# Performance work log

Hardware: AMD Instinct MI355X
Metric: run time of the kernel (lower is better)

## Reference

```python
import jax, jax.numpy as jnp
import numpy as np

B, S, D, H = 2, 2048, 1024, 16
DK = D // H

def setup_inputs() -> dict:
    key = jax.random.key(0)
    ks = jax.random.split(key, 12)
    def lin(k, shape, fan_in):
        bound = 1.0 / np.sqrt(fan_in)
        return jax.random.uniform(k, shape, jnp.float32, -bound, bound)
    inp = {
        'Q': jax.random.normal(ks[0], (B, S, D), jnp.float32),
        'K': jax.random.normal(ks[1], (B, S, D), jnp.float32),
        'V': jax.random.normal(ks[2], (B, S, D), jnp.float32),
        # padding mask: last 128 key positions of batch element 0 are padding
        'padding_mask': jnp.ones((B, 1, 1, S), jnp.int32).at[0, :, :, -128:].set(0),
        # causal look-ahead mask
        'look_ahead_mask': jnp.tril(jnp.ones((S, S), jnp.int32))[None, None],
        'Wq': lin(ks[3], (D, D), D), 'bq': lin(ks[4], (D,), D),
        'Wk': lin(ks[5], (D, D), D), 'bk': lin(ks[6], (D,), D),
        'Wv': lin(ks[7], (D, D), D), 'bv': lin(ks[8], (D,), D),
        'Wo': lin(ks[9], (D, D), D), 'bo': lin(ks[10], (D,), D),
    }
    return inp

def _split_heads(x):
    # [B,S,D] -> [B,H,S,DK]
    b, s, _ = x.shape
    return x.reshape(b, s, H, DK).transpose(0, 2, 1, 3)

def reference(Q, K, V, padding_mask, look_ahead_mask, Wq, bq, Wk, bk, Wv, bv, Wo, bo):
    q = _split_heads(Q @ Wq.T + bq)  # [B,H,S,DK]
    k = _split_heads(K @ Wk.T + bk)
    v = _split_heads(V @ Wv.T + bv)
    scores = jnp.einsum('bhqd,bhkd->bhqk', q, k) / np.sqrt(DK).astype(np.float32)
    neg_inf = jnp.float32(-jnp.inf)
    scores = jnp.where(padding_mask == 0, neg_inf, scores)
    scores = jnp.where(look_ahead_mask == 0, neg_inf, scores)
    weights = jax.nn.softmax(scores, axis=-1)  # dropout is identity in eval mode
    x = jnp.einsum('bhqk,bhkd->bhqd', weights, v)  # [B,H,S,DK]
    x = x.transpose(0, 2, 1, 3).reshape(Q.shape[0], Q.shape[1], D)
    return x @ Wo.T + bo
```

## Files before the change

### kernel.cpp

```cpp
#include <hip/hip_runtime.h>
#include <hip/hip_bf16.h>

#define B_   2
#define S_   2048
#define D_   1024
#define H_   16
#define DK_  64

typedef unsigned short u16;
typedef __attribute__((ext_vector_type(8))) short bf16x8;
typedef __attribute__((ext_vector_type(4))) float f32x4;

#define CHUNK_   12
#define NSLOT_   48

static __device__ __forceinline__ u16 f2bf(float f) {
  union { float f; unsigned u; } v; v.f = f;
  unsigned r = v.u + 0x7FFF + ((v.u >> 16) & 1);
  return (u16)(r >> 16);
}

static __device__ __forceinline__ void gl_lds16(const void* g, void* l) {
  __builtin_amdgcn_global_load_lds(
      (const __attribute__((address_space(1))) void*)g,
      (__attribute__((address_space(3))) void*)l, 16, 0, 0);
}

__global__ void cvt7(const float4* __restrict__ i0, const float4* __restrict__ i1,
                     const float4* __restrict__ i2, const float4* __restrict__ i3,
                     const float4* __restrict__ i4, const float4* __restrict__ i5,
                     const float4* __restrict__ i6,
                     ushort4* __restrict__ o0, ushort4* __restrict__ o1,
                     ushort4* __restrict__ o2, ushort4* __restrict__ o3,
                     ushort4* __restrict__ o4, ushort4* __restrict__ o5,
                     ushort4* __restrict__ o6, int nbig, int nsmall) {
  int y = blockIdx.y;
  const float4* in; ushort4* out; int bound;
  switch (y) {
    case 0: in = i0; out = o0; bound = nbig; break;
    case 1: in = i1; out = o1; bound = nbig; break;
    case 2: in = i2; out = o2; bound = nbig; break;
    case 3: in = i3; out = o3; bound = nsmall; break;
    case 4: in = i4; out = o4; bound = nsmall; break;
    case 5: in = i5; out = o5; bound = nsmall; break;
    default: in = i6; out = o6; bound = nsmall; break;
  }
  int i = blockIdx.x * blockDim.x + threadIdx.x;
  if (i < bound) {
    float4 v = in[i];
    ushort4 r;
    r.x = f2bf(v.x); r.y = f2bf(v.y); r.z = f2bf(v.z); r.w = f2bf(v.w);
    out[i] = r;
  }
}

__launch_bounds__(256, 3)
__global__ void gemm_qkv(const u16* __restrict__ Xq, const u16* __restrict__ Xk, const u16* __restrict__ Xv,
                         const u16* __restrict__ Wq, const u16* __restrict__ Wk, const u16* __restrict__ Wv,
                         const float* __restrict__ bq, const float* __restrict__ bk, const float* __restrict__ bv,
                         u16* __restrict__ outq, u16* __restrict__ outk, u16* __restrict__ outv) {
  const int z = blockIdx.z;
  const u16* Am; const u16* Bm; int m0, n0;
  if (z == 2) { Am = Wv; Bm = Xv; m0 = blockIdx.x * 128; n0 = blockIdx.y * 128; }
  else if (z == 1) { Am = Xk; Bm = Wk; m0 = blockIdx.y * 128; n0 = blockIdx.x * 128; }
  else { Am = Xq; Bm = Wq; m0 = blockIdx.y * 128; n0 = blockIdx.x * 128; }
  const float* bias = (z == 0) ? bq : (z == 1) ? bk : bv;

  __shared__ __align__(16) u16 As[128 * 64];
  __shared__ __align__(16) u16 Bs[128 * 64];

  const int tid = threadIdx.x, lane = tid & 63, w = tid >> 6;
  const int q = lane >> 4, cl = lane & 15;
  const int wr = w >> 1, wc = w & 1;

  f32x4 acc[4][4] = {};

  for (int k0 = 0; k0 < D_; k0 += 64) {
#pragma unroll
    for (int i = 0; i < 4; ++i) {
      int ch = i * 256 + tid;
      int row = ch >> 3, c = ch & 7;
      int gc = (c ^ (row & 7)) << 3;
      gl_lds16(Am + (size_t)(m0 + row) * D_ + k0 + gc, As + ch * 8);
      gl_lds16(Bm + (size_t)(n0 + row) * D_ + k0 + gc, Bs + ch * 8);
    }
    __syncthreads();

#pragma unroll
    for (int kk = 0; kk < 2; ++kk) {
      bf16x8 af[4], bfr[4];
      int jc = (kk << 2) | q;
#pragma unroll
      for (int r = 0; r < 4; ++r)
        af[r]  = *(const bf16x8*)(As + (wr * 64 + r * 16 + cl) * 64 + ((jc ^ (cl & 7)) << 3));
#pragma unroll
      for (int c = 0; c < 4; ++c)
        bfr[c] = *(const bf16x8*)(Bs + (wc * 64 + c * 16 + cl) * 64 + ((jc ^ (cl & 7)) << 3));
#pragma unroll
      for (int r = 0; r < 4; ++r)
#pragma unroll
        for (int c = 0; c < 4; ++c)
          acc[r][c] = __builtin_amdgcn_mfma_f32_16x16x32_bf16(af[r], bfr[c], acc[r][c], 0, 0, 0);
    }
    __syncthreads();
  }

  if (z == 2) {
#pragma unroll
    for (int r = 0; r < 4; ++r) {
#pragma unroll
      for (int rr = 0; rr < 4; ++rr) {
        int j = m0 + wr * 64 + r * 16 + q * 4 + rr;
        float bval = bias[j];
        int hh = j >> 6, dk = j & 63;
#pragma unroll
        for (int c = 0; c < 4; ++c) {
          int n = n0 + wc * 64 + c * 16 + cl;
          int bb = n >> 11, s = n & (S_ - 1);
          outv[((size_t)(bb * H_ + hh) * DK_ + dk) * S_ + s] = f2bf(acc[r][c][rr] + bval);
        }
      }
    }
  } else {
    const float scale = (z == 0) ? 0.125f : 1.0f;
    u16* o = (z == 0) ? outq : outk;
#pragma unroll
    for (int c = 0; c < 4; ++c) {
      int j = n0 + wc * 64 + c * 16 + cl;
      float bval = bias[j];
      int hh = j >> 6, dk = j & 63;
#pragma unroll
      for (int r = 0; r < 4; ++r) {
#pragma unroll
        for (int rr = 0; rr < 4; ++rr) {
          int n = m0 + wr * 64 + r * 16 + q * 4 + rr;
          int bb = n >> 11, s = n & (S_ - 1);
          o[((size_t)(bb * H_ + hh) * S_ + s) * DK_ + dk] = f2bf((acc[r][c][rr] + bval) * scale);
        }
      }
    }
  }
}

__launch_bounds__(256, 4)
__global__ void attn(const u16* __restrict__ qh, const u16* __restrict__ kh,
                     const u16* __restrict__ vt, const int* __restrict__ pad,
                     u16* __restrict__ attn_out, float* __restrict__ Po, float* __restrict__ Pl) {
  __shared__ __align__(16) u16 Ks[64 * 64];
  __shared__ __align__(16) u16 Vs[64 * 64];
  __shared__ __align__(16) u16 Ps[4][16 * 72];
  __shared__ float Kbias[64];

  const int tid = threadIdx.x, lane = tid & 63, w = tid >> 6;
  const int q = lane >> 4, cl = lane & 15;
  const int h = blockIdx.y, b = blockIdx.z;

  const int x = blockIdx.x;
  int qt, ch, nch;
  if (x < 24)      { qt = 24 + x / 3;          ch = x % 3;       nch = 3; }
  else if (x < 48) { int y = x - 24; qt = 12 + y / 2; ch = y & 1; nch = 2; }
  else             { qt = x - 48;              ch = 0;           nch = 1; }
  const int qb = qt * 64;
  const int t0 = ch * CHUNK_;
  const int t1 = (qt < t0 + CHUNK_ - 1) ? qt : (t0 + CHUNK_ - 1);

  const u16* Q = qh + (size_t)(b * H_ + h) * S_ * DK_;
  const u16* K = kh + (size_t)(b * H_ + h) * S_ * DK_;
  const u16* V = vt + (size_t)(b * H_ + h) * DK_ * S_;
  const int* pm = pad + b * S_;

  const int qr0 = qb + w * 16;
  bf16x8 qf0 = *(const bf16x8*)(Q + (qr0 + cl) * DK_ + q * 8);
  bf16x8 qf1 = *(const bf16x8*)(Q + (qr0 + cl) * DK_ + 32 + q * 8);

  f32x4 o[4] = {};
  float ls[4] = {0.f, 0.f, 0.f, 0.f};
  u16* Pw = Ps[w];

  for (int it = t0; it <= t1; ++it) {
    const int kb = it << 6;
#pragma unroll
    for (int i = 0; i < 2; ++i) {
      int s = (i * 4 + w) * 64 + lane;
      int row = s >> 3;
      int c = (s & 7) ^ (row & 7);
      gl_lds16(K + (size_t)(kb + row) * DK_ + (c << 3), Ks + (size_t)s * 8);
      gl_lds16(V + (size_t)row * S_ + kb + (c << 3), Vs + (size_t)s * 8);
    }
    if (tid < 64) {
      Kbias[tid] = (pm[kb + tid] != 0) ? -6.0f : -3e38f;
    }
    __syncthreads();

    f32x4 sa[4];
#pragma unroll
    for (int ct = 0; ct < 4; ++ct) {
      int rk = ct * 16 + cl;
      int c0 = q ^ (rk & 7);
      bf16x8 kf0 = *(const bf16x8*)(Ks + rk * 64 + (c0 << 3));
      bf16x8 kf1 = *(const bf16x8*)(Ks + rk * 64 + ((c0 ^ 4) << 3));
      f32x4 zz = {};
      zz = __builtin_amdgcn_mfma_f32_16x16x32_bf16(qf0, kf0, zz, 0, 0, 0);
      zz = __builtin_amdgcn_mfma_f32_16x16x32_bf16(qf1, kf1, zz, 0, 0, 0);
      sa[ct] = zz;
    }

    if (it < qt) {
#pragma unroll
      for (int ct = 0; ct < 4; ++ct) {
        float kbv = Kbias[ct * 16 + cl];
#pragma unroll
        for (int rr = 0; rr < 4; ++rr) {
          float p = __expf(sa[ct][rr] + kbv);
          ls[rr] += p;
          Pw[(q * 4 + rr) * 72 + ct * 16 + cl] = f2bf(p);
        }
      }
    } else {
#pragma unroll
      for (int ct = 0; ct < 4; ++ct) {
        int kg = kb + ct * 16 + cl;
        float kbv = Kbias[ct * 16 + cl];
#pragma unroll
        for (int rr = 0; rr < 4; ++rr) {
          int qg = qr0 + q * 4 + rr;
          float p = (kg <= qg) ? __expf(sa[ct][rr] + kbv) : 0.f;
          ls[rr] += p;
          Pw[(q * 4 + rr) * 72 + ct * 16 + cl] = f2bf(p);
        }
      }
    }

    bf16x8 pf0 = *(const bf16x8*)(Pw + cl * 72 + q * 8);
    bf16x8 pf1 = *(const bf16x8*)(Pw + cl * 72 + 32 + q * 8);

#pragma unroll
    for (int ct = 0; ct < 4; ++ct) {
      int rv = ct * 16 + cl;
      int c0 = q ^ (rv & 7);
      bf16x8 vf0 = *(const bf16x8*)(Vs + rv * 64 + (c0 << 3));
      bf16x8 vf1 = *(const bf16x8*)(Vs + rv * 64 + ((c0 ^ 4) << 3));
      o[ct] = __builtin_amdgcn_mfma_f32_16x16x32_bf16(pf0, vf0, o[ct], 0, 0, 0);
      o[ct] = __builtin_amdgcn_mfma_f32_16x16x32_bf16(pf1, vf1, o[ct], 0, 0, 0);
    }
    __syncthreads();
  }

  if (nch == 1) {
#pragma unroll
    for (int rr = 0; rr < 4; ++rr) {
      float l = ls[rr];
      l += __shfl_xor(l, 1, 64);
      l += __shfl_xor(l, 2, 64);
      l += __shfl_xor(l, 4, 64);
      l += __shfl_xor(l, 8, 64);
      float inv = 1.0f / l;
      int qg = qr0 + q * 4 + rr;
      size_t base = (size_t)(b * S_ + qg) * D_ + h * DK_;
#pragma unroll
      for (int ct = 0; ct < 4; ++ct)
        attn_out[base + ct * 16 + cl] = f2bf(o[ct][rr] * inv);
    }
  } else {
    int pq = qt - 12;
    int off = (pq < 12) ? pq * 2 : 24 + (pq - 12) * 3;
    size_t slot = (size_t)(b * H_ + h) * NSLOT_ + off + ch;
#pragma unroll
    for (int rr = 0; rr < 4; ++rr) {
      float l = ls[rr];
      l += __shfl_xor(l, 1, 64);
      l += __shfl_xor(l, 2, 64);
      l += __shfl_xor(l, 4, 64);
      l += __shfl_xor(l, 8, 64);
      int rl = w * 16 + q * 4 + rr;
      if (cl == 0) Pl[slot * 64 + rl] = l;
      float* po = Po + ((size_t)slot * 64 + rl) * 64;
#pragma unroll
      for (int ct = 0; ct < 4; ++ct)
        po[ct * 16 + cl] = o[ct][rr];
    }
  }
}

__global__ void combine(const float* __restrict__ Po, const float* __restrict__ Pl,
                        u16* __restrict__ attn_out) {
  const int qt = 12 + blockIdx.x, h = blockIdx.y, b = blockIdx.z;
  const int nch = (qt < 24) ? 2 : 3;
  const int pq = qt - 12;
  const int off = (pq < 12) ? pq * 2 : 24 + (pq - 12) * 3;
  const size_t slot0 = (size_t)(b * H_ + h) * NSLOT_ + off;

  const int c = threadIdx.x & 63;
  const int r0 = (threadIdx.x >> 6) * 16;
#pragma unroll 4
  for (int i = 0; i < 16; ++i) {
    int r = r0 + i;
    float os = 0.f, lsum = 0.f;
    for (int ch = 0; ch < nch; ++ch) {
      os += Po[((slot0 + ch) * 64 + r) * 64 + c];
      lsum += Pl[(slot0 + ch) * 64 + r];
    }
    int qg = qt * 64 + r;
    attn_out[(size_t)(b * S_ + qg) * D_ + h * DK_ + c] = f2bf(os / lsum);
  }
}

__launch_bounds__(256, 3)
__global__ void gemm_out(const u16* __restrict__ A, const u16* __restrict__ W,
                         const float* __restrict__ bias, float* __restrict__ out) {
  __shared__ __align__(16) u16 As[128 * 64];
  __shared__ __align__(16) u16 Bs[128 * 64];

  const int tid = threadIdx.x, lane = tid & 63, w = tid >> 6;
  const int q = lane >> 4, cl = lane & 15;
  const int wr = w >> 1, wc = w & 1;
  const int m0 = blockIdx.y * 128, n0 = blockIdx.x * 128;

  f32x4 acc[4][4] = {};

  for (int k0 = 0; k0 < D_; k0 += 64) {
#pragma unroll
    for (int i = 0; i < 4; ++i) {
      int ch = i * 256 + tid;
      int row = ch >> 3, c = ch & 7;
      int gc = (c ^ (row & 7)) << 3;
      gl_lds16(A + (size_t)(m0 + row) * D_ + k0 + gc, As + ch * 8);
      gl_lds16(W + (size_t)(n0 + row) * D_ + k0 + gc, Bs + ch * 8);
    }
    __syncthreads();

#pragma unroll
    for (int kk = 0; kk < 2; ++kk) {
      bf16x8 af[4], bfr[4];
      int jc = (kk << 2) | q;
#pragma unroll
      for (int r = 0; r < 4; ++r)
        af[r]  = *(const bf16x8*)(As + (wr * 64 + r * 16 + cl) * 64 + ((jc ^ (cl & 7)) << 3));
#pragma unroll
      for (int c = 0; c < 4; ++c)
        bfr[c] = *(const bf16x8*)(Bs + (wc * 64 + c * 16 + cl) * 64 + ((jc ^ (cl & 7)) << 3));
#pragma unroll
      for (int r = 0; r < 4; ++r)
#pragma unroll
        for (int c = 0; c < 4; ++c)
          acc[r][c] = __builtin_amdgcn_mfma_f32_16x16x32_bf16(af[r], bfr[c], acc[r][c], 0, 0, 0);
    }
    __syncthreads();
  }

#pragma unroll
  for (int c = 0; c < 4; ++c) {
    int j = n0 + wc * 64 + c * 16 + cl;
    float bval = bias[j];
#pragma unroll
    for (int r = 0; r < 4; ++r) {
#pragma unroll
      for (int rr = 0; rr < 4; ++rr) {
        int n = m0 + wr * 64 + r * 16 + q * 4 + rr;
        out[(size_t)n * D_ + j] = acc[r][c][rr] + bval;
      }
    }
  }
}

extern "C" void kernel_launch(void* const* d_in, const int* in_sizes, int n_in,
                              void* d_out, int out_size, void* d_ws, size_t ws_size,
                              hipStream_t stream) {
  const float* Qf  = (const float*)d_in[0];
  const float* Kf  = (const float*)d_in[1];
  const float* Vf  = (const float*)d_in[2];
  const int*   pad = (const int*)d_in[3];
  const float* Wqf = (const float*)d_in[5];
  const float* bq  = (const float*)d_in[6];
  const float* Wkf = (const float*)d_in[7];
  const float* bk  = (const float*)d_in[8];
  const float* Wvf = (const float*)d_in[9];
  const float* bv  = (const float*)d_in[10];
  const float* Wof = (const float*)d_in[11];
  const float* bo  = (const float*)d_in[12];

  const size_t BSD = (size_t)B_ * S_ * D_;
  const size_t DD  = (size_t)D_ * D_;

  char* ws = (char*)d_ws;
  u16* Qb   = (u16*)ws; ws += BSD * 2;
  u16* Kb   = (u16*)ws; ws += BSD * 2;
  u16* Vb   = (u16*)ws; ws += BSD * 2;
  u16* Wqb  = (u16*)ws; ws += DD * 2;
  u16* Wkb  = (u16*)ws; ws += DD * 2;
  u16* Wvb  = (u16*)ws; ws += DD * 2;
  u16* Wob  = (u16*)ws; ws += DD * 2;
  u16* qhd  = (u16*)ws; ws += BSD * 2;
  u16* khd  = (u16*)ws; ws += BSD * 2;
  u16* vtd  = (u16*)ws; ws += BSD * 2;
  u16* attn_o = (u16*)ws; ws += BSD * 2;

  float* Po = (float*)d_ws;
  float* Pl = Po + (size_t)B_ * H_ * NSLOT_ * 64 * 64;

  const int n4 = (int)(BSD / 4);
  const int w4 = (int)(DD / 4);
  dim3 gc(n4 / 256, 7);
  cvt7<<<gc, 256, 0, stream>>>((const float4*)Qf, (const float4*)Kf, (const float4*)Vf,
                               (const float4*)Wqf, (const float4*)Wkf, (const float4*)Wvf, (const float4*)Wof,
                               (ushort4*)Qb, (ushort4*)Kb, (ushort4*)Vb,
                               (ushort4*)Wqb, (ushort4*)Wkb, (ushort4*)Wvb, (ushort4*)Wob, n4, w4);

  dim3 g1(D_ / 128, (B_ * S_) / 128, 3);
  gemm_qkv<<<g1, 256, 0, stream>>>(Qb, Kb, Vb, Wqb, Wkb, Wvb, bq, bk, bv, qhd, khd, vtd);

  dim3 g2(60, H_, B_);
  attn<<<g2, 256, 0, stream>>>(qhd, khd, vtd, pad, attn_o, Po, Pl);

  dim3 g2b(20, H_, B_);
  combine<<<g2b, 256, 0, stream>>>(Po, Pl, attn_o);

  dim3 g3(D_ / 128, (B_ * S_) / 128);
  gemm_out<<<g3, 256, 0, stream>>>(attn_o, Wob, bo, (float*)d_out);
}
```

Baseline: 255.9 us.

## Double-buffer K tiles, load V directly to registers, widen combine grid

The attention kernel now double-buffers the K tile in LDS, prefetching the next tile during the current iteration, and drops one barrier per iteration. V fragments are loaded straight from global memory into registers instead of being staged through LDS, and the padding-mask bias is read per lane rather than through shared memory. This lowers LDS use and raises the occupancy hint from 4 to 5. The combine kernel is flattened to one element per thread with a 16x larger grid, which trades its per-thread loop for more parallelism. Direct global V loads may be less coalesced and add latency that the MFMA work has to hide.

```diff
diff --git a/kernel.cpp b/kernel.cpp
--- a/kernel.cpp
+++ b/kernel.cpp
@@ -142,14 +142,12 @@
   }
 }
 
-__launch_bounds__(256, 4)
+__launch_bounds__(256, 5)
 __global__ void attn(const u16* __restrict__ qh, const u16* __restrict__ kh,
                      const u16* __restrict__ vt, const int* __restrict__ pad,
                      u16* __restrict__ attn_out, float* __restrict__ Po, float* __restrict__ Pl) {
-  __shared__ __align__(16) u16 Ks[64 * 64];
-  __shared__ __align__(16) u16 Vs[64 * 64];
+  __shared__ __align__(16) u16 Ks[2][64 * 64];
   __shared__ __align__(16) u16 Ps[4][16 * 72];
-  __shared__ float Kbias[64];
 
   const int tid = threadIdx.x, lane = tid & 63, w = tid >> 6;
   const int q = lane >> 4, cl = lane & 15;
@@ -177,28 +175,58 @@
   float ls[4] = {0.f, 0.f, 0.f, 0.f};
   u16* Pw = Ps[w];
 
+  const int s_ch0 = w * 64 + lane;
+  const int s_ch1 = (4 + w) * 64 + lane;
+
+  {
+    const int kb = t0 << 6;
+#pragma unroll
+    for (int i = 0; i < 2; ++i) {
+      int s = (i == 0) ? s_ch0 : s_ch1;
+      int row = s >> 3;
+      int c = (s & 7) ^ (row & 7);
+      gl_lds16(K + (size_t)(kb + row) * DK_ + (c << 3), Ks[0] + (size_t)s * 8);
+    }
+  }
+  __syncthreads();
+
+  int cur = 0;
   for (int it = t0; it <= t1; ++it) {
     const int kb = it << 6;
-#pragma unroll
-    for (int i = 0; i < 2; ++i) {
-      int s = (i * 4 + w) * 64 + lane;
-      int row = s >> 3;
-      int c = (s & 7) ^ (row & 7);
-      gl_lds16(K + (size_t)(kb + row) * DK_ + (c << 3), Ks + (size_t)s * 8);
-      gl_lds16(V + (size_t)row * S_ + kb + (c << 3), Vs + (size_t)s * 8);
-    }
-    if (tid < 64) {
-      Kbias[tid] = (pm[kb + tid] != 0) ? -6.0f : -3e38f;
-    }
-    __syncthreads();
+
+    bf16x8 vf0[4], vf1[4];
+#pragma unroll
+    for (int ct = 0; ct < 4; ++ct) {
+      const u16* Vr = V + (size_t)(ct * 16 + cl) * S_ + kb + q * 8;
+      vf0[ct] = *(const bf16x8*)(Vr);
+      vf1[ct] = *(const bf16x8*)(Vr + 32);
+    }
+
+    if (it < t1) {
+      const int kb1 = kb + 64;
+#pragma unroll
+      for (int i = 0; i < 2; ++i) {
+        int s = (i == 0) ? s_ch0 : s_ch1;
+        int row = s >> 3;
+        int c = (s & 7) ^ (row & 7);
+        gl_lds16(K + (size_t)(kb1 + row) * DK_ + (c << 3), Ks[cur ^ 1] + (size_t)s * 8);
+      }
+    }
+
+    float kbv[4];
+#pragma unroll
+    for (int ct = 0; ct < 4; ++ct)
+      kbv[ct] = (pm[kb + ct * 16 + cl] != 0) ? -6.0f : -3e38f;
+
+    const u16* Kc = Ks[cur];
 
     f32x4 sa[4];
 #pragma unroll
     for (int ct = 0; ct < 4; ++ct) {
       int rk = ct * 16 + cl;
       int c0 = q ^ (rk & 7);
-      bf16x8 kf0 = *(const bf16x8*)(Ks + rk * 64 + (c0 << 3));
-      bf16x8 kf1 = *(const bf16x8*)(Ks + rk * 64 + ((c0 ^ 4) << 3));
+      bf16x8 kf0 = *(const bf16x8*)(Kc + rk * 64 + (c0 << 3));
+      bf16x8 kf1 = *(const bf16x8*)(Kc + rk * 64 + ((c0 ^ 4) << 3));
       f32x4 zz = {};
       zz = __builtin_amdgcn_mfma_f32_16x16x32_bf16(qf0, kf0, zz, 0, 0, 0);
       zz = __builtin_amdgcn_mfma_f32_16x16x32_bf16(qf1, kf1, zz, 0, 0, 0);
@@ -208,10 +236,9 @@
     if (it < qt) {
 #pragma unroll
       for (int ct = 0; ct < 4; ++ct) {
-        float kbv = Kbias[ct * 16 + cl];
 #pragma unroll
         for (int rr = 0; rr < 4; ++rr) {
-          float p = __expf(sa[ct][rr] + kbv);
+          float p = __expf(sa[ct][rr] + kbv[ct]);
           ls[rr] += p;
           Pw[(q * 4 + rr) * 72 + ct * 16 + cl] = f2bf(p);
         }
@@ -220,11 +247,10 @@
 #pragma unroll
       for (int ct = 0; ct < 4; ++ct) {
         int kg = kb + ct * 16 + cl;
-        float kbv = Kbias[ct * 16 + cl];
 #pragma unroll
         for (int rr = 0; rr < 4; ++rr) {
           int qg = qr0 + q * 4 + rr;
-          float p = (kg <= qg) ? __expf(sa[ct][rr] + kbv) : 0.f;
+          float p = (kg <= qg) ? __expf(sa[ct][rr] + kbv[ct]) : 0.f;
           ls[rr] += p;
           Pw[(q * 4 + rr) * 72 + ct * 16 + cl] = f2bf(p);
         }
@@ -236,14 +262,12 @@
 
 #pragma unroll
     for (int ct = 0; ct < 4; ++ct) {
-      int rv = ct * 16 + cl;
-      int c0 = q ^ (rv & 7);
-      bf16x8 vf0 = *(const bf16x8*)(Vs + rv * 64 + (c0 << 3));
-      bf16x8 vf1 = *(const bf16x8*)(Vs + rv * 64 + ((c0 ^ 4) << 3));
-      o[ct] = __builtin_amdgcn_mfma_f32_16x16x32_bf16(pf0, vf0, o[ct], 0, 0, 0);
-      o[ct] = __builtin_amdgcn_mfma_f32_16x16x32_bf16(pf1, vf1, o[ct], 0, 0, 0);
-    }
+      o[ct] = __builtin_amdgcn_mfma_f32_16x16x32_bf16(pf0, vf0[ct], o[ct], 0, 0, 0);
+      o[ct] = __builtin_amdgcn_mfma_f32_16x16x32_bf16(pf1, vf1[ct], o[ct], 0, 0, 0);
+    }
+
     __syncthreads();
+    cur ^= 1;
   }
 
   if (nch == 1) {
@@ -284,25 +308,23 @@
 
 __global__ void combine(const float* __restrict__ Po, const float* __restrict__ Pl,
                         u16* __restrict__ attn_out) {
-  const int qt = 12 + blockIdx.x, h = blockIdx.y, b = blockIdx.z;
+  const int x = blockIdx.x, h = blockIdx.y, b = blockIdx.z;
+  const int qt = 12 + (x >> 4);
+  const int inner = ((x & 15) << 8) + threadIdx.x;
+  const int r = inner >> 6, c = inner & 63;
+
   const int nch = (qt < 24) ? 2 : 3;
   const int pq = qt - 12;
   const int off = (pq < 12) ? pq * 2 : 24 + (pq - 12) * 3;
   const size_t slot0 = (size_t)(b * H_ + h) * NSLOT_ + off;
 
-  const int c = threadIdx.x & 63;
-  const int r0 = (threadIdx.x >> 6) * 16;
-#pragma unroll 4
-  for (int i = 0; i < 16; ++i) {
-    int r = r0 + i;
-    float os = 0.f, lsum = 0.f;
-    for (int ch = 0; ch < nch; ++ch) {
-      os += Po[((slot0 + ch) * 64 + r) * 64 + c];
-      lsum += Pl[(slot0 + ch) * 64 + r];
-    }
-    int qg = qt * 64 + r;
-    attn_out[(size_t)(b * S_ + qg) * D_ + h * DK_ + c] = f2bf(os / lsum);
-  }
+  float os = 0.f, lsum = 0.f;
+  for (int ch = 0; ch < nch; ++ch) {
+    os += Po[((slot0 + ch) * 64 + r) * 64 + c];
+    lsum += Pl[(slot0 + ch) * 64 + r];
+  }
+  int qg = qt * 64 + r;
+  attn_out[(size_t)(b * S_ + qg) * D_ + h * DK_ + c] = f2bf(os / lsum);
 }
 
 __launch_bounds__(256, 3)
@@ -412,7 +434,7 @@
   dim3 g2(60, H_, B_);
   attn<<<g2, 256, 0, stream>>>(qhd, khd, vtd, pad, attn_o, Po, Pl);
 
-  dim3 g2b(20, H_, B_);
+  dim3 g2b(320, H_, B_);
   combine<<<g2b, 256, 0, stream>>>(Po, Pl, attn_o);
 
   dim3 g3(D_ / 128, (B_ * S_) / 128);
```

New measurement: 364.5 us. 42.5% more time.
